# Performance work log

Measured on AMD Instinct MI355X. Metric: run time of the kernel, lower is better.

Reference implementation:

```python
import math
import jax, jax.numpy as jnp
import numpy as np

B = 1024
D = 384
Q = 65536
TOPK = 128
HARD_W = 2.0
TEMP_START = 0.2
TEMP_END = 0.05
WARMUP = 10


def _temperature(epoch):
    # curriculum cosine decay (epoch is a Python int)
    if epoch >= WARMUP:
        return TEMP_END
    progress = epoch / max(1, WARMUP)
    return TEMP_END + 0.5 * (TEMP_START - TEMP_END) * (1.0 + math.cos(math.pi * progress))


def _normalize(x):
    # F.normalize: x / max(||x||, eps)
    n = jnp.linalg.norm(x, axis=-1, keepdims=True)
    return x / jnp.maximum(n, 1e-12)


def _hard_neg_reweight(logits):
    # logits: [B, N]; labels = arange(B) (diagonal positives)
    b = logits.shape[0]
    rows = jnp.arange(b)
    neg_logits = logits.at[rows, rows].set(-jnp.inf)      # mask positives
    _, hard_idx = jax.lax.top_k(neg_logits, TOPK)          # [B, TOPK] hardest negatives
    weights = jnp.ones_like(logits)
    weights = weights.at[rows[:, None], hard_idx].set(HARD_W)
    weights = weights.at[rows, rows].set(1.0)
    return logits * weights


def _cross_entropy_diag(logits):
    b = logits.shape[0]
    logp = jax.nn.log_softmax(logits, axis=-1)
    return -jnp.mean(logp[jnp.arange(b), jnp.arange(b)])


def setup_inputs() -> dict:
    key = jax.random.key(0)
    k1, k2, k3, k4 = jax.random.split(key, 4)
    rgb_feat = jax.random.normal(k1, (B, D), dtype=jnp.float32)
    ir_feat = jax.random.normal(k2, (B, D), dtype=jnp.float32)
    rgb_queue = _normalize(jax.random.normal(k3, (Q, D), dtype=jnp.float32))
    ir_queue = _normalize(jax.random.normal(k4, (Q, D), dtype=jnp.float32))
    return {"rgb_feat": rgb_feat, "ir_feat": ir_feat,
            "rgb_queue": rgb_queue, "ir_queue": ir_queue, "epoch": 0}


def reference(rgb_feat, ir_feat, rgb_queue, ir_queue, epoch):
    temp = _temperature(epoch)
    rgb_z = _normalize(rgb_feat.astype(jnp.float32))
    ir_z = _normalize(ir_feat.astype(jnp.float32))
    ir_all = jnp.concatenate([ir_z, ir_queue], axis=0)    # [B+Q, D]
    rgb_all = jnp.concatenate([rgb_z, rgb_queue], axis=0)
    logits_r2i = (rgb_z @ ir_all.T) / temp                # [B, B+Q]
    logits_i2r = (ir_z @ rgb_all.T) / temp
    logits_r2i = _hard_neg_reweight(logits_r2i)
    logits_i2r = _hard_neg_reweight(logits_i2r)
    return 0.5 * (_cross_entropy_diag(logits_r2i) + _cross_entropy_diag(logits_i2r))
```

## Files before the change

### kernel.cpp

```cpp
#include <hip/hip_runtime.h>
#include <hip/hip_bf16.h>

#define B_    1024
#define D_    384
#define Q_    65536
#define N_    66560
#define TOPK_ 128

#define NBIN_ 4096
#define CAP_  2048
#define SRANK_ 24
#define SLOTS_ 17

typedef __bf16 bf16x8 __attribute__((ext_vector_type(8)));
typedef float  f32x4  __attribute__((ext_vector_type(4)));
typedef unsigned short u16;
typedef u16 u16x8 __attribute__((ext_vector_type(8)));

__device__ __forceinline__ unsigned short f2bf(float x) {
  unsigned int u = __float_as_uint(x);
  unsigned int r = (u + 0x7fffu + ((u >> 16) & 1u)) >> 16;
  return (unsigned short)r;
}

__device__ __forceinline__ void gld_lds16(const void* g, void* l) {
  __builtin_amdgcn_global_load_lds(
      (__attribute__((address_space(1))) void*)(g),
      (__attribute__((address_space(3))) void*)(l), 16, 0, 0);
}

__device__ __forceinline__ void wait_vmcnt(int n) {
  switch (n) {
    case 4:  asm volatile("s_waitcnt vmcnt(4)"  ::: "memory"); break;
    default: asm volatile("s_waitcnt vmcnt(0)"  ::: "memory"); break;
  }
}

__device__ __forceinline__ unsigned int bf2key(unsigned int u) {
  return u ^ ((u & 0x8000u) ? 0xFFFFu : 0x8000u);
}
__device__ __forceinline__ float key2val(unsigned int k) {
  unsigned int u = (k & 0x8000u) ? (k ^ 0x8000u) : (~k & 0xFFFFu);
  return __uint_as_float(u << 16);
}

__global__ __launch_bounds__(64) void k_normalize(
    const float* __restrict__ rgb, const float* __restrict__ ir,
    const int* __restrict__ ep,
    u16* __restrict__ zrA, u16* __restrict__ ziA,
    u16* __restrict__ zrU, u16* __restrict__ ziU)
{
  int r = blockIdx.x & (B_ - 1);
  bool isIr = blockIdx.x >= B_;
  const float* src = (isIr ? ir : rgb) + (size_t)r * D_;
  u16* dA = (isIr ? ziA : zrA) + (size_t)r * D_;
  u16* dU = (isIr ? ziU : zrU) + (size_t)r * D_;
  int t = threadIdx.x;
  float x[6]; float ss = 0.f;
  #pragma unroll
  for (int k = 0; k < 6; ++k) { x[k] = src[t + 64*k]; ss += x[k]*x[k]; }
  #pragma unroll
  for (int off = 32; off > 0; off >>= 1) ss += __shfl_down(ss, off);
  ss = __shfl(ss, 0);
  float inv = 1.0f / fmaxf(sqrtf(ss), 1e-12f);

  int e = ep[0];
  float temp;
  if (e >= 10) temp = 0.05f;
  else {
    float p = (float)e * 0.1f;
    temp = 0.05f + 0.075f * (1.0f + cosf(3.14159265358979323846f * p));
  }
  float itemp = 1.0f / temp;

  #pragma unroll
  for (int k = 0; k < 6; ++k) {
    float z = x[k] * inv;
    dU[t + 64*k] = f2bf(z);
    dA[t + 64*k] = f2bf(z * itemp);
  }
}

__global__ __launch_bounds__(256) void k_build_ball(
    const u16* __restrict__ zU, const float* __restrict__ queue,
    u16* __restrict__ ball)
{
  size_t i = ((size_t)blockIdx.x * 256 + threadIdx.x) * 8;
  const size_t zElems = (size_t)B_ * D_;
  if (i < zElems) {
    *(uint4*)(ball + i) = *(const uint4*)(zU + i);
  } else {
    const float* q = queue + (i - zElems);
    float4 a = *(const float4*)q;
    float4 b = *(const float4*)(q + 4);
    u16x8 o;
    o[0] = f2bf(a.x); o[1] = f2bf(a.y); o[2] = f2bf(a.z); o[3] = f2bf(a.w);
    o[4] = f2bf(b.x); o[5] = f2bf(b.y); o[6] = f2bf(b.z); o[7] = f2bf(b.w);
    *(u16x8*)(ball + i) = o;
  }
}

#define BK_ 32
#define NSTEP_ 12
__global__ __launch_bounds__(256, 3) void k_gemm(
    const u16* __restrict__ A,
    const u16* __restrict__ ball,
    u16* __restrict__ C,
    float* __restrict__ diag,
    int r0, int mtiles)
{
  __shared__ __align__(16) unsigned char smem[49152];
  u16* Ct = (u16*)smem;

  int bid = blockIdx.x;
  int nwg = gridDim.x;
  int cpx = nwg >> 3;
  int wgid = (bid & 7) * cpx + (bid >> 3);
  int nt = wgid / mtiles;
  int mt = wgid - nt * mtiles;

  const int tid  = threadIdx.x;
  const int wave = tid >> 6, lane = tid & 63;
  const int wm = wave >> 1, wn = wave & 1;
  const int mbase = mt * 128;
  const int nbase = nt * 128;
  const u16* Ab = A    + (size_t)(r0 + mbase) * D_;
  const u16* Bb = ball + (size_t)nbase * D_;

  auto As = [&](int t) -> u16* { return (u16*)(smem + (t % 3) * 16384); };
  auto Bs = [&](int t) -> u16* { return (u16*)(smem + (t % 3) * 16384 + 8192); };
  auto stage = [&](int t) {
    const int ks = t * BK_;
    #pragma unroll
    for (int i = 0; i < 2; ++i) {
      int f = i * 256 + tid;
      int rr = f >> 2, cc = f & 3;
      int koff = (((cc * 16) ^ (((rr >> 1) & 3) << 4)) >> 1);
      gld_lds16(Ab + (size_t)rr * D_ + ks + koff, As(t) + (size_t)f * 8);
      gld_lds16(Bb + (size_t)rr * D_ + ks + koff, Bs(t) + (size_t)f * 8);
    }
  };

  f32x4 acc[4][4];
  #pragma unroll
  for (int m = 0; m < 4; ++m)
    #pragma unroll
    for (int n = 0; n < 4; ++n)
      #pragma unroll
      for (int r = 0; r < 4; ++r) acc[m][n][r] = 0.0f;

  const int lr = lane & 15;
  const int kb = (lane >> 4) * 16;

  stage(0); stage(1);

  #pragma unroll
  for (int t = 0; t < NSTEP_; ++t) {
    wait_vmcnt(t < NSTEP_ - 1 ? 4 : 0);
    __builtin_amdgcn_s_barrier();
    __builtin_amdgcn_sched_barrier(0);

    const u16* Ac = As(t);
    const u16* Bc = Bs(t);
    bf16x8 af[4], bq[4];
    #pragma unroll
    for (int m = 0; m < 4; ++m) {
      int row = wm*64 + m*16 + lr;
      af[m] = *(const bf16x8*)((const char*)Ac + row * 64 + (kb ^ (((row >> 1) & 3) << 4)));
    }
    #pragma unroll
    for (int n = 0; n < 4; ++n) {
      int row = wn*64 + n*16 + lr;
      bq[n] = *(const bf16x8*)((const char*)Bc + row * 64 + (kb ^ (((row >> 1) & 3) << 4)));
    }
    if (t + 2 < NSTEP_) stage(t + 2);

    #pragma unroll
    for (int m = 0; m < 4; ++m)
      #pragma unroll
      for (int n = 0; n < 4; ++n)
        acc[m][n] = __builtin_amdgcn_mfma_f32_16x16x32_bf16(af[m], bq[n], acc[m][n], 0, 0, 0);

    asm volatile("s_waitcnt lgkmcnt(0)" ::: "memory");
    __builtin_amdgcn_sched_barrier(0);
  }
  __syncthreads();

  const int rowq = (lane >> 4) * 4;
  #pragma unroll
  for (int m = 0; m < 4; ++m) {
    #pragma unroll
    for (int n = 0; n < 4; ++n) {
      int lcol = wn*64 + n*16 + lr;
      int gcol = nbase + lcol;
      #pragma unroll
      for (int r = 0; r < 4; ++r) {
        int lrow = wm*64 + m*16 + rowq + r;
        float x = acc[m][n][r];
        int grow = r0 + mbase + lrow;
        if (gcol == grow) { diag[grow] = x; x = -60.0f; }
        Ct[lrow * 136 + lcol] = f2bf(x);
      }
    }
  }
  __syncthreads();

  int rrow = tid >> 4;
  int cchunk = (tid & 15) * 8;
  #pragma unroll
  for (int pass = 0; pass < 8; ++pass) {
    int row = pass * 16 + rrow;
    u16x8 v = *(const u16x8*)(Ct + row * 136 + cchunk);
    *(u16x8*)(C + (size_t)(mbase + row) * N_ + nbase + cchunk) = v;
  }
}

__global__ __launch_bounds__(256) void k_select(
    const u16* __restrict__ C, const float* __restrict__ diag,
    float* __restrict__ rowloss, int r0)
{
  __shared__ unsigned int hist[NBIN_];
  __shared__ u16 keyslots[256 * SLOTS_];
  __shared__ float vals[CAP_];
  __shared__ float fred[256];
  __shared__ unsigned int csum[256];
  __shared__ int lcnt[256];
  __shared__ unsigned int subhist[16];
  __shared__ float sh_d2;
  __shared__ int shv[4];

  const int t = threadIdx.x;
  const int grow = r0 + blockIdx.x;
  const u16x8* p = (const u16x8*)(C + (size_t)blockIdx.x * N_);

  uint4* h4 = (uint4*)hist;
  #pragma unroll
  for (int i = 0; i < 4; ++i) h4[i * 256 + t] = make_uint4(0,0,0,0);
  if (t < 16) subhist[t] = 0;
  if (t == 0) { shv[2] = 0; sh_d2 = 0.f; }
  __syncthreads();

  {
    u16x8 s0 = p[t * 32];
    u16x8 s1 = p[t * 32 + 16];
    #pragma unroll
    for (int e = 0; e < 8; ++e) {
      atomicAdd(&hist[bf2key((unsigned int)(unsigned short)s0[e]) >> 4], 1u);
      atomicAdd(&hist[bf2key((unsigned int)(unsigned short)s1[e]) >> 4], 1u);
    }
  }
  __syncthreads();
  {
    unsigned int S = 0;
    #pragma unroll
    for (int i = 0; i < 16; ++i) S += hist[t * 16 + i];
    csum[t] = S;
    __syncthreads();
    unsigned int a = S;
    #pragma unroll
    for (int s = 1; s < 256; s <<= 1) {
      unsigned int add = (t + s < 256) ? csum[t + s] : 0u;
      __syncthreads();
      a += add; csum[t] = a;
      __syncthreads();
    }
    int above = (t < 255) ? (int)csum[t + 1] : 0;
    if (above < SRANK_ && above + (int)S >= SRANK_) {
      int cum = above;
      #pragma unroll 1
      for (int i = 15; i >= 0; --i) {
        int c = (int)hist[t * 16 + i];
        if (cum + c >= SRANK_) { shv[3] = t * 16 + i; break; }
        cum += c;
      }
    }
  }
  __syncthreads();
  const unsigned int tfine = (unsigned int)shv[3];
  #pragma unroll
  for (int i = 0; i < 4; ++i) h4[i * 256 + t] = make_uint4(0,0,0,0);
  __syncthreads();

  u16* myslots = keyslots + t * SLOTS_;
  int lc = 0;
  float es0 = 0.f, es1 = 0.f;
  #pragma unroll 1
  for (int base = 0; base < 8192; base += 2048) {
    u16x8 v[8];
    #pragma unroll
    for (int j = 0; j < 8; ++j) v[j] = p[base + j * 256 + t];
    #pragma unroll
    for (int j = 0; j < 8; ++j) {
      #pragma unroll
      for (int e = 0; e < 8; ++e) {
        unsigned int u = (unsigned int)(unsigned short)v[j][e];
        unsigned int k = bf2key(u);
        unsigned int bin = k >> 4;
        atomicAdd(&hist[bin], 1u);
        float ex = __expf(__uint_as_float(u << 16));
        if (j & 1) es1 += ex; else es0 += ex;
        myslots[lc < 16 ? lc : 16] = (u16)k;
        lc += (bin >= tfine);
      }
    }
  }
  if (t < 128) {
    u16x8 v = p[8192 + t];
    #pragma unroll
    for (int e = 0; e < 8; ++e) {
      unsigned int u = (unsigned int)(unsigned short)v[e];
      unsigned int k = bf2key(u);
      unsigned int bin = k >> 4;
      atomicAdd(&hist[bin], 1u);
      es0 += __expf(__uint_as_float(u << 16));
      myslots[lc < 16 ? lc : 16] = (u16)k;
      lc += (bin >= tfine);
    }
  }
  float esum = es0 + es1;
  lcnt[t] = lc;
  __syncthreads();

  unsigned int S = 0;
  #pragma unroll
  for (int i = 0; i < 16; ++i) S += hist[t * 16 + i];
  csum[t] = S;
  __syncthreads();
  unsigned int a = S;
  #pragma unroll
  for (int s = 1; s < 256; s <<= 1) {
    unsigned int add = (t + s < 256) ? csum[t + s] : 0u;
    __syncthreads();
    a += add; csum[t] = a;
    __syncthreads();
  }

  int above_chunk = (t < 255) ? (int)csum[t + 1] : 0;
  if (above_chunk < TOPK_ && above_chunk + (int)S >= TOPK_) {
    int cum = above_chunk;
    #pragma unroll 1
    for (int i = 15; i >= 0; --i) {
      int c = (int)hist[t * 16 + i];
      if (cum + c >= TOPK_) { shv[0] = t * 16 + i; shv[1] = cum; break; }
      cum += c;
    }
  }
  int ok_lc = __syncthreads_and(lc <= 16);
  const unsigned int bstar = (unsigned int)shv[0];
  const int A = shv[1];
  const int need0 = TOPK_ - A;

  float delta = 0.f;
  if (ok_lc && bstar >= tfine) {
    #pragma unroll 1
    for (int i = t; i < 256 * 16; i += 256) {
      int ts = i >> 4, sl = i & 15;
      int c = lcnt[ts]; c = c < 16 ? c : 16;
      if (sl < c) {
        unsigned int k = (unsigned int)keyslots[ts * SLOTS_ + sl];
        unsigned int bin = k >> 4;
        if (bin > bstar) {
          float v = key2val(k);
          delta += __expf(2.f * v) - __expf(v);
        } else if (bin == bstar) {
          atomicAdd(&subhist[k & 15], 1u);
        }
      }
    }
    __syncthreads();
    if (t == 0) {
      int need = need0; float d2 = 0.f;
      #pragma unroll 1
      for (int sk = 15; sk >= 0 && need > 0; --sk) {
        int c = (int)subhist[sk];
        if (c > 0) {
          int take = c < need ? c : need;
          float v = key2val((bstar << 4) | (unsigned int)sk);
          d2 += (float)take * (__expf(2.f * v) - __expf(v));
          need -= take;
        }
      }
      sh_d2 = d2;
    }
  } else {
    if (t == 0) shv[2] = 0;
    __syncthreads();
    #pragma unroll 1
    for (int base = 0; base < 8192; base += 2048) {
      u16x8 v[8];
      #pragma unroll
      for (int j = 0; j < 8; ++j) v[j] = p[base + j * 256 + t];
      #pragma unroll
      for (int j = 0; j < 8; ++j) {
        #pragma unroll
        for (int e = 0; e < 8; ++e) {
          unsigned int u = (unsigned int)(unsigned short)v[j][e];
          unsigned int bin = bf2key(u) >> 4;
          if (bin >= bstar) {
            float val = __uint_as_float(u << 16);
            if (bin > bstar) delta += __expf(2.f * val) - __expf(val);
            else { int s = atomicAdd(&shv[2], 1); if (s < CAP_) vals[s] = val; }
          }
        }
      }
    }
    if (t < 128) {
      u16x8 v = p[8192 + t];
      #pragma unroll
      for (int e = 0; e < 8; ++e) {
        unsigned int u = (unsigned int)(unsigned short)v[e];
        unsigned int bin = bf2key(u) >> 4;
        if (bin >= bstar) {
          float val = __uint_as_float(u << 16);
          if (bin > bstar) delta += __expf(2.f * val) - __expf(val);
          else { int s = atomicAdd(&shv[2], 1); if (s < CAP_) vals[s] = val; }
        }
      }
    }
    __syncthreads();
    int C2 = shv[2] < CAP_ ? shv[2] : CAP_;
    for (int i = t; i < C2; i += 256) {
      float v = vals[i];
      int g = 0;
      for (int k = 0; k < C2; ++k)
        g += (vals[k] > v) || (vals[k] == v && k < i);
      if (g < need0) delta += __expf(2.f * v) - __expf(v);
    }
  }

  fred[t] = esum + delta;
  __syncthreads();
  #pragma unroll
  for (int s = 128; s > 0; s >>= 1) { if (t < s) fred[t] += fred[t + s]; __syncthreads(); }

  if (t == 0) {
    float d = diag[grow];
    rowloss[grow] = logf(fred[0] + sh_d2 + __expf(d)) - d;
  }
}

__global__ __launch_bounds__(256) void k_final(
    const float* __restrict__ rowloss, float* __restrict__ out)
{
  __shared__ float red[256];
  int t = threadIdx.x;
  float s = 0.f;
  for (int i = t; i < 2 * B_; i += 256) s += rowloss[i];
  red[t] = s;
  __syncthreads();
  for (int k = 128; k > 0; k >>= 1) { if (t < k) red[t] += red[t + k]; __syncthreads(); }
  if (t == 0) out[0] = red[0] * (1.0f / (2.0f * B_));
}

extern "C" void kernel_launch(void* const* d_in, const int* in_sizes, int n_in,
                              void* d_out, int out_size, void* d_ws, size_t ws_size,
                              hipStream_t stream)
{
  const float* rgb_feat = (const float*)d_in[0];
  const float* ir_feat  = (const float*)d_in[1];
  const float* rgb_q    = (const float*)d_in[2];
  const float* ir_q     = (const float*)d_in[3];
  const int*   epoch    = (const int*)d_in[4];

  char* ws = (char*)d_ws;
  size_t off = 0;
  auto alloc = [&](size_t bytes) -> char* {
    char* p = ws + off;
    off = (off + bytes + 255) & ~(size_t)255;
    return p;
  };

  u16* zrA = (u16*)alloc((size_t)B_ * D_ * 2);
  u16* ziA = (u16*)alloc((size_t)B_ * D_ * 2);
  u16* zrU = (u16*)alloc((size_t)B_ * D_ * 2);
  u16* ziU = (u16*)alloc((size_t)B_ * D_ * 2);
  float* diag    = (float*)alloc((size_t)2 * B_ * 4);
  float* rowloss = (float*)alloc((size_t)2 * B_ * 4);
  u16* ball = (u16*)alloc((size_t)N_ * D_ * 2);

  size_t avail = ws_size > off ? ws_size - off : 0;
  int SR = (int)(avail / ((size_t)N_ * 2));
  SR &= ~127;
  if (SR > B_) SR = B_;
  if (SR < 128) SR = 128;
  u16* slab = (u16*)(ws + off);

  k_normalize<<<dim3(2 * B_), dim3(64), 0, stream>>>(
      rgb_feat, ir_feat, epoch, zrA, ziA, zrU, ziU);

  for (int dir = 0; dir < 2; ++dir) {
    const u16*   Amat   = (dir == 0) ? zrA : ziA;
    const u16*   zOther = (dir == 0) ? ziU : zrU;
    const float* queue  = (dir == 0) ? ir_q : rgb_q;
    float* diagD = diag    + dir * B_;
    float* lossD = rowloss + dir * B_;

    k_build_ball<<<dim3((unsigned)((size_t)N_ * D_ / 8 / 256)), dim3(256), 0, stream>>>(
        zOther, queue, ball);

    for (int r0 = 0; r0 < B_; r0 += SR) {
      int cur = (B_ - r0) < SR ? (B_ - r0) : SR;
      int mtiles = cur / 128;
      int nwg = (N_ / 128) * mtiles;
      k_gemm<<<dim3(nwg), dim3(256), 0, stream>>>(
          Amat, ball, slab, diagD, r0, mtiles);
      k_select<<<dim3(cur), dim3(256), 0, stream>>>(slab, diagD, lossD, r0);
    }
  }

  k_final<<<dim3(1), dim3(256), 0, stream>>>(rowloss, (float*)d_out);
}
```

Baseline: 305.2 us.

## Build histogram only from pre-filtered candidate keys in the fast path

The full-row LDS histogram with per-element atomics is removed from the main pass. The kernel first reduces per-thread candidate counts (keys at or above a precomputed fine threshold). If all candidates fit in the slots and there are at least TOPK of them, it builds the histogram only from those stored keys. Otherwise it falls back to a second full pass that builds the complete histogram. This removes about 66K shared atomics per row in the common case, at the cost of an extra reduction and a slower fallback path.

```diff
diff --git a/kernel.cpp b/kernel.cpp
--- a/kernel.cpp
+++ b/kernel.cpp
@@ -295,12 +295,10 @@
       for (int e = 0; e < 8; ++e) {
         unsigned int u = (unsigned int)(unsigned short)v[j][e];
         unsigned int k = bf2key(u);
-        unsigned int bin = k >> 4;
-        atomicAdd(&hist[bin], 1u);
         float ex = __expf(__uint_as_float(u << 16));
         if (j & 1) es1 += ex; else es0 += ex;
         myslots[lc < 16 ? lc : 16] = (u16)k;
-        lc += (bin >= tfine);
+        lc += ((k >> 4) >= tfine);
       }
     }
   }
@@ -310,48 +308,66 @@
     for (int e = 0; e < 8; ++e) {
       unsigned int u = (unsigned int)(unsigned short)v[e];
       unsigned int k = bf2key(u);
-      unsigned int bin = k >> 4;
-      atomicAdd(&hist[bin], 1u);
       es0 += __expf(__uint_as_float(u << 16));
       myslots[lc < 16 ? lc : 16] = (u16)k;
-      lc += (bin >= tfine);
+      lc += ((k >> 4) >= tfine);
     }
   }
   float esum = es0 + es1;
   lcnt[t] = lc;
   __syncthreads();
 
-  unsigned int S = 0;
-  #pragma unroll
-  for (int i = 0; i < 16; ++i) S += hist[t * 16 + i];
-  csum[t] = S;
-  __syncthreads();
-  unsigned int a = S;
-  #pragma unroll
-  for (int s = 1; s < 256; s <<= 1) {
-    unsigned int add = (t + s < 256) ? csum[t + s] : 0u;
-    __syncthreads();
-    a += add; csum[t] = a;
-    __syncthreads();
-  }
-
-  int above_chunk = (t < 255) ? (int)csum[t + 1] : 0;
-  if (above_chunk < TOPK_ && above_chunk + (int)S >= TOPK_) {
-    int cum = above_chunk;
+  {
+    unsigned int a = (unsigned int)lcnt[t];
+    csum[t] = a;
+    __syncthreads();
+    #pragma unroll
+    for (int s = 128; s > 0; s >>= 1) {
+      unsigned int add = (t < s) ? csum[t + s] : 0u;
+      __syncthreads();
+      if (t < s) csum[t] = csum[t] + add;
+      __syncthreads();
+    }
+  }
+  const int cntTot = (int)csum[0];
+  int ok_lc = __syncthreads_and(lc <= 16);
+
+  float delta = 0.f;
+  if (ok_lc && cntTot >= TOPK_) {
     #pragma unroll 1
-    for (int i = 15; i >= 0; --i) {
-      int c = (int)hist[t * 16 + i];
-      if (cum + c >= TOPK_) { shv[0] = t * 16 + i; shv[1] = cum; break; }
-      cum += c;
-    }
-  }
-  int ok_lc = __syncthreads_and(lc <= 16);
-  const unsigned int bstar = (unsigned int)shv[0];
-  const int A = shv[1];
-  const int need0 = TOPK_ - A;
-
-  float delta = 0.f;
-  if (ok_lc && bstar >= tfine) {
+    for (int i = t; i < 256 * 16; i += 256) {
+      int ts = i >> 4, sl = i & 15;
+      int c = lcnt[ts]; c = c < 16 ? c : 16;
+      if (sl < c)
+        atomicAdd(&hist[(unsigned int)keyslots[ts * SLOTS_ + sl] >> 4], 1u);
+    }
+    __syncthreads();
+    unsigned int S = 0;
+    #pragma unroll
+    for (int i = 0; i < 16; ++i) S += hist[t * 16 + i];
+    csum[t] = S;
+    __syncthreads();
+    unsigned int a = S;
+    #pragma unroll
+    for (int s = 1; s < 256; s <<= 1) {
+      unsigned int add = (t + s < 256) ? csum[t + s] : 0u;
+      __syncthreads();
+      a += add; csum[t] = a;
+      __syncthreads();
+    }
+    int above_chunk = (t < 255) ? (int)csum[t + 1] : 0;
+    if (above_chunk < TOPK_ && above_chunk + (int)S >= TOPK_) {
+      int cum = above_chunk;
+      #pragma unroll 1
+      for (int i = 15; i >= 0; --i) {
+        int c = (int)hist[t * 16 + i];
+        if (cum + c >= TOPK_) { shv[0] = t * 16 + i; shv[1] = cum; break; }
+        cum += c;
+      }
+    }
+    __syncthreads();
+    const unsigned int bstar = (unsigned int)shv[0];
+    const int need0 = TOPK_ - shv[1];
     #pragma unroll 1
     for (int i = t; i < 256 * 16; i += 256) {
       int ts = i >> 4, sl = i & 15;
@@ -383,8 +399,50 @@
       sh_d2 = d2;
     }
   } else {
-    if (t == 0) shv[2] = 0;
-    __syncthreads();
+    #pragma unroll 1
+    for (int base = 0; base < 8192; base += 2048) {
+      u16x8 v[8];
+      #pragma unroll
+      for (int j = 0; j < 8; ++j) v[j] = p[base + j * 256 + t];
+      #pragma unroll
+      for (int j = 0; j < 8; ++j)
+        #pragma unroll
+        for (int e = 0; e < 8; ++e)
+          atomicAdd(&hist[bf2key((unsigned int)(unsigned short)v[j][e]) >> 4], 1u);
+    }
+    if (t < 128) {
+      u16x8 v = p[8192 + t];
+      #pragma unroll
+      for (int e = 0; e < 8; ++e)
+        atomicAdd(&hist[bf2key((unsigned int)(unsigned short)v[e]) >> 4], 1u);
+    }
+    __syncthreads();
+    unsigned int S = 0;
+    #pragma unroll
+    for (int i = 0; i < 16; ++i) S += hist[t * 16 + i];
+    csum[t] = S;
+    __syncthreads();
+    unsigned int a = S;
+    #pragma unroll
+    for (int s = 1; s < 256; s <<= 1) {
+      unsigned int add = (t + s < 256) ? csum[t + s] : 0u;
+      __syncthreads();
+      a += add; csum[t] = a;
+      __syncthreads();
+    }
+    int above_chunk = (t < 255) ? (int)csum[t + 1] : 0;
+    if (above_chunk < TOPK_ && above_chunk + (int)S >= TOPK_) {
+      int cum = above_chunk;
+      #pragma unroll 1
+      for (int i = 15; i >= 0; --i) {
+        int c = (int)hist[t * 16 + i];
+        if (cum + c >= TOPK_) { shv[0] = t * 16 + i; shv[1] = cum; break; }
+        cum += c;
+      }
+    }
+    __syncthreads();
+    const unsigned int bstar = (unsigned int)shv[0];
+    const int need0 = TOPK_ - shv[1];
     #pragma unroll 1
     for (int base = 0; base < 8192; base += 2048) {
       u16x8 v[8];
```

After: 298.8 us (median of 5 runs). -2.1%, faster.
